# Optimization experiments

Hardware: AMD Instinct MI355X
Metric: run time of the kernel (lower is better)

## Reference

```python
import jax, jax.numpy as jnp
import numpy as np

NUM_HEADS = 12

def setup_inputs() -> dict:
    key = jax.random.key(0)
    ks = jax.random.split(key, 5)
    B, S, E = 1, 4096, 768
    x = jax.random.normal(ks[0], (B, S, E), dtype=jnp.float32)
    Wqkv = jax.random.normal(ks[1], (3 * E, E), dtype=jnp.float32) * (E ** -0.5)
    bqkv = jax.random.normal(ks[2], (3 * E,), dtype=jnp.float32) * 0.02
    Wo = jax.random.normal(ks[3], (E, E), dtype=jnp.float32) * (E ** -0.5)
    bo = jax.random.normal(ks[4], (E,), dtype=jnp.float32) * 0.02
    return {"x": x, "Wqkv": Wqkv, "bqkv": bqkv, "Wo": Wo, "bo": bo, "window_size": 128}

def reference(x, Wqkv, bqkv, Wo, bo, window_size):
    B, S, E = x.shape
    H = NUM_HEADS
    hd = E // H
    # qkv projection: [B,S,3E] -> [B,S,H,3*hd] -> split
    qkv = (x @ Wqkv.T + bqkv).reshape(B, S, H, 3 * hd)
    q, k, v = jnp.split(qkv, 3, axis=-1)  # each [B,S,H,hd]
    q = q.transpose(0, 2, 1, 3)  # [B,H,S,hd]
    k = k.transpose(0, 2, 1, 3)
    v = v.transpose(0, 2, 1, 3)
    # dense scores, masked to local window |i-j| <= window_size
    scores = jnp.einsum('bhqd,bhkd->bhqk', q, k) / (hd ** 0.5)
    idx = jnp.arange(S)
    in_window = jnp.abs(idx[:, None] - idx[None, :]) <= window_size  # [S,S]
    scores = jnp.where(in_window[None, None, :, :], scores, -jnp.inf)
    attn = jax.nn.softmax(scores, axis=-1)
    out = jnp.einsum('bhqk,bhkd->bhqd', attn, v)  # [B,H,S,hd]
    out = out.transpose(0, 2, 1, 3).reshape(B, S, E)
    return out @ Wo.T + bo
```

## Files before the change

### kernel.cpp

```cpp
#include <hip/hip_runtime.h>


typedef __attribute__((ext_vector_type(8))) short short8;
typedef __attribute__((ext_vector_type(4))) short short4v;
typedef __attribute__((ext_vector_type(4))) float f32x4;

#define S_LEN 4096
#define EMB   768
#define NH    12
#define HD    64
#define QT    64
#define WMAX  128
#define NKT   20
#define QSCALE 0.18033688f

#if defined(__HIP_DEVICE_COMPILE__)
#define MFMA16(a, b, c) __builtin_amdgcn_mfma_f32_16x16x16bf16_1k(a, b, c, 0, 0, 0)
#else
#define MFMA16(a, b, c) (c)
#endif

__device__ __forceinline__ short f2bf(float f) {
    union { unsigned int i; float f; } c;
    c.f = f;
    unsigned int i = c.i;
    unsigned int r = (i + 0x7FFFu + ((i >> 16) & 1u)) >> 16;
    return (short)(unsigned short)r;
}

#define NX4  (S_LEN * EMB / 4)
#define NW4  (3 * EMB * EMB / 4)
#define NO4  (EMB * EMB / 4)
__global__ __launch_bounds__(256) void convert_all(
    const float* __restrict__ x, const float* __restrict__ wqkv,
    const float* __restrict__ wo, short* __restrict__ xb,
    short* __restrict__ wqkvb, short* __restrict__ wob)
{
    int base = blockIdx.x * 1024 + threadIdx.x;
#pragma unroll
    for (int p = 0; p < 4; ++p) {
        int i = base + p * 256;
        const float* src; short* dst; int off;
        if (i < NX4)            { src = x;    dst = xb;    off = i; }
        else if (i < NX4 + NW4) { src = wqkv; dst = wqkvb; off = i - NX4; }
        else                    { src = wo;   dst = wob;   off = i - NX4 - NW4; }
        float4 v = ((const float4*)src)[off];
        short4v o = { f2bf(v.x), f2bf(v.y), f2bf(v.z), f2bf(v.w) };
        *(short4v*)(dst + (size_t)off * 4) = o;
    }
}

__global__ __launch_bounds__(256) void gemm_qkv(
    const short* __restrict__ A, const short* __restrict__ B,
    const float* __restrict__ bias, short* __restrict__ Cv,
    int M, int N, int K)
{
    __shared__ __align__(16) short smem[2 * 4096 + 2 * 3072];
    short* As0 = smem;
    short* Bs0 = smem + 2 * 4096;

    const int t = threadIdx.x;
    const int w = t >> 6, l = t & 63;
    const int quad = l >> 4, lane16 = l & 15;
    const int m0 = blockIdx.y * 128, n0 = blockIdx.x * 96;
    const int wm = (w >> 1) * 64, wn = (w & 1) * 48;

    f32x4 acc[4][3];
#pragma unroll
    for (int i = 0; i < 4; ++i)
#pragma unroll
        for (int j = 0; j < 3; ++j) acc[i][j] = (f32x4){0.f, 0.f, 0.f, 0.f};

    const int NKI = K >> 5;

    auto stage = [&](int ki, int b) {
        short* Asb = As0 + b * 4096;
        short* Bsb = Bs0 + b * 3072;
#pragma unroll
        for (int i = 0; i < 4; ++i) {
            int c = i * 256 + t;
            if (c < 512) {
                int r = c >> 2, kc = c & 3;
#if defined(__HIP_DEVICE_COMPILE__) && __has_builtin(__builtin_amdgcn_global_load_lds)
                __builtin_amdgcn_global_load_lds(
                    (const __attribute__((address_space(1))) void*)(A + (size_t)(m0 + r) * K + ki * 32 + kc * 8),
                    (__attribute__((address_space(3))) void*)(Asb + c * 8), 16, 0, 0);
#else
                *(short8*)(Asb + c * 8) = *(const short8*)(A + (size_t)(m0 + r) * K + ki * 32 + kc * 8);
#endif
            } else if (c < 896) {
                int cb = c - 512;
                int r = cb >> 2, kc = cb & 3;
#if defined(__HIP_DEVICE_COMPILE__) && __has_builtin(__builtin_amdgcn_global_load_lds)
                __builtin_amdgcn_global_load_lds(
                    (const __attribute__((address_space(1))) void*)(B + (size_t)(n0 + r) * K + ki * 32 + kc * 8),
                    (__attribute__((address_space(3))) void*)(Bsb + cb * 8), 16, 0, 0);
#else
                *(short8*)(Bsb + cb * 8) = *(const short8*)(B + (size_t)(n0 + r) * K + ki * 32 + kc * 8);
#endif
            }
        }
    };

    stage(0, 0);
    for (int kb = 0; kb < NKI; ++kb) {
        const int cur = kb & 1;
        __syncthreads();
        if (kb + 1 < NKI) stage(kb + 1, cur ^ 1);

        const short* Asb = As0 + cur * 4096;
        const short* Bsb = Bs0 + cur * 3072;
        short8 af[4], bfr[3];
#pragma unroll
        for (int mt = 0; mt < 4; ++mt)
            af[mt] = *(const short8*)(Asb + (wm + mt * 16 + lane16) * 32 + quad * 8);
#pragma unroll
        for (int nt = 0; nt < 3; ++nt)
            bfr[nt] = *(const short8*)(Bsb + (wn + nt * 16 + lane16) * 32 + quad * 8);
#pragma unroll
        for (int mt = 0; mt < 4; ++mt)
#pragma unroll
            for (int nt = 0; nt < 3; ++nt)
                acc[mt][nt] = __builtin_amdgcn_mfma_f32_16x16x32_bf16(
                    af[mt], bfr[nt], acc[mt][nt], 0, 0, 0);
    }

    __syncthreads();
    short(*Ct)[100] = (short(*)[100])smem;

#pragma unroll
    for (int nt = 0; nt < 3; ++nt) {
        int col = n0 + wn + nt * 16 + lane16;
        float bv = bias[col];
        int h = col / 192;
        int rem = col - h * 192;
        int ty = rem >> 6, d = rem & 63;
        if (ty == 2) {
            short* vt = Cv + ((size_t)2 * NH * S_LEN) * HD + ((size_t)h * HD + d) * S_LEN;
#pragma unroll
            for (int mt = 0; mt < 4; ++mt) {
                int row0 = m0 + wm + mt * 16 + quad * 4;
                short4v o = { f2bf(acc[mt][nt][0] + bv), f2bf(acc[mt][nt][1] + bv),
                              f2bf(acc[mt][nt][2] + bv), f2bf(acc[mt][nt][3] + bv) };
                *(short4v*)(vt + row0) = o;
            }
        } else {
            float s = (ty == 0) ? QSCALE : 1.f;
            int cl = wn + nt * 16 + lane16;
#pragma unroll
            for (int mt = 0; mt < 4; ++mt) {
#pragma unroll
                for (int r = 0; r < 4; ++r)
                    Ct[wm + mt * 16 + quad * 4 + r][cl] = f2bf((acc[mt][nt][r] + bv) * s);
            }
        }
    }
    __syncthreads();

#pragma unroll
    for (int pass = 0; pass < 6; ++pass) {
        int c = pass * 256 + t;
        int row = c / 12, cg = c - row * 12;
        int col0 = n0 + cg * 8;
        int h = col0 / 192;
        int rem = col0 - h * 192;
        int ty = rem >> 6;
        if (ty == 2) continue;
        int d0 = rem - ty * 64;
        short* dst = Cv + (((size_t)ty * NH + h) * S_LEN + (m0 + row)) * HD + d0;
        *(short8*)dst = *(const short8*)(&Ct[row][cg * 8]);
    }
}

__global__ __launch_bounds__(256, 3) void attn_win(
    const short* __restrict__ qsplit, const int* __restrict__ wptr,
    short* __restrict__ attn_out)
{
    __shared__ __align__(16) short KS[320 * 64];

    const int t = threadIdx.x;
    const int w = t >> 6, l = t & 63;
    const int quad = l >> 4, lane16 = l & 15;

    const int id = blockIdx.x;
    const int xcd = id & 7, j = id >> 3;
    const int h = j >> 3;
    const int q0 = ((xcd << 3) + (j & 7)) * QT;
    const int W = *wptr;
    const int kbase = q0 - WMAX;

    const short* Qh  = qsplit + (size_t)h * S_LEN * HD;
    const short* Kh  = qsplit + (size_t)(NH + h) * S_LEN * HD;
    const short* VtG = qsplit + (size_t)2 * NH * S_LEN * HD + (size_t)h * HD * S_LEN;

#pragma unroll
    for (int i = 0; i < 10; ++i) {
        int c = i * 256 + t;
        int r = c >> 3, gs = c & 7;
        int g = gs ^ (r & 7);
        int idx = min(max(kbase + r, 0), S_LEN - 1);
#if defined(__HIP_DEVICE_COMPILE__) && __has_builtin(__builtin_amdgcn_global_load_lds)
        __builtin_amdgcn_global_load_lds(
            (const __attribute__((address_space(1))) void*)(Kh + (size_t)idx * HD + g * 8),
            (__attribute__((address_space(3))) void*)(KS + c * 8), 16, 0, 0);
#else
        *(short8*)(KS + c * 8) = *(const short8*)(Kh + (size_t)idx * HD + g * 8);
#endif
    }
    const int qi = q0 + w * 16 + lane16;
    const short* qp = Qh + (size_t)qi * HD;
    short8 bq0 = *(const short8*)(qp + quad * 8);
    short8 bq1 = *(const short8*)(qp + 32 + quad * 8);

    __syncthreads();

    f32x4 sc[NKT];
    const int d7 = lane16 & 7;
    const int s0 = (quad ^ d7) * 8;
    const int s1 = ((quad + 4) ^ d7) * 8;
#pragma unroll
    for (int kt = 0; kt < NKT; ++kt) {
        const short* kp = KS + (kt * 16 + lane16) * 64;
        short8 a0 = *(const short8*)(kp + s0);
        short8 a1 = *(const short8*)(kp + s1);
        f32x4 a = (f32x4){0.f, 0.f, 0.f, 0.f};
        a = __builtin_amdgcn_mfma_f32_16x16x32_bf16(a0, bq0, a, 0, 0, 0);
        a = __builtin_amdgcn_mfma_f32_16x16x32_bf16(a1, bq1, a, 0, 0, 0);
        sc[kt] = a;
    }

    __syncthreads();

#pragma unroll
    for (int i = 0; i < 10; ++i) {
        int c = i * 256 + t;
        int d = c / 40;
        int slot = c - d * 40;
        int sg = slot >> 3, s = slot & 7;
        int g = s ^ (d & 7);
        int key0 = kbase + sg * 64 + g * 8;
        key0 = min(max(key0, 0), S_LEN - 8);
#if defined(__HIP_DEVICE_COMPILE__) && __has_builtin(__builtin_amdgcn_global_load_lds)
        __builtin_amdgcn_global_load_lds(
            (const __attribute__((address_space(1))) void*)(VtG + (size_t)d * S_LEN + key0),
            (__attribute__((address_space(3))) void*)(KS + c * 8), 16, 0, 0);
#else
        *(short8*)(KS + c * 8) = *(const short8*)(VtG + (size_t)d * S_LEN + key0);
#endif
    }

    float m = -1e30f;
#pragma unroll
    for (int kt = 0; kt < NKT; ++kt) {
#pragma unroll
        for (int r = 0; r < 4; ++r) {
            int key = kbase + kt * 16 + quad * 4 + r;
            int dd = qi - key;
            int ad = dd < 0 ? -dd : dd;
            bool valid = ((unsigned)key < S_LEN) && (ad <= W);
            float s = valid ? sc[kt][r] : -1e30f;
            sc[kt][r] = s;
            m = fmaxf(m, s);
        }
    }
    m = fmaxf(m, __shfl_xor(m, 16, 64));
    m = fmaxf(m, __shfl_xor(m, 32, 64));

    float lsum = 0.f;
#pragma unroll
    for (int kt = 0; kt < NKT; ++kt) {
#pragma unroll
        for (int r = 0; r < 4; ++r) {
            float p = exp2f(sc[kt][r] - m);
            sc[kt][r] = p;
            lsum += p;
        }
    }
    lsum += __shfl_xor(lsum, 16, 64);
    lsum += __shfl_xor(lsum, 32, 64);
    const float rl = 1.f / fmaxf(lsum, 1e-30f);

    __syncthreads();

    f32x4 oacc[4];
#pragma unroll
    for (int nt = 0; nt < 4; ++nt) oacc[nt] = (f32x4){0.f, 0.f, 0.f, 0.f};

#pragma unroll
    for (int kt = 0; kt < NKT; ++kt) {
        short4v pb = { f2bf(sc[kt][0]), f2bf(sc[kt][1]),
                       f2bf(sc[kt][2]), f2bf(sc[kt][3]) };
        int G = kt * 2 + (quad >> 1);
        int off = (G >> 3) * 64 + ((G & 7) ^ d7) * 8 + (quad & 1) * 4;
#pragma unroll
        for (int nt = 0; nt < 4; ++nt) {
            short4v va = *(const short4v*)(KS + (nt * 16 + lane16) * 320 + off);
            oacc[nt] = MFMA16(va, pb, oacc[nt]);
        }
    }

#pragma unroll
    for (int nt = 0; nt < 4; ++nt) {
        short4v ob = { f2bf(oacc[nt][0] * rl), f2bf(oacc[nt][1] * rl),
                       f2bf(oacc[nt][2] * rl), f2bf(oacc[nt][3] * rl) };
        *(short4v*)(attn_out + (size_t)qi * EMB + h * HD + nt * 16 + quad * 4) = ob;
    }
}

__global__ __launch_bounds__(256) void gemm_out96(
    const short* __restrict__ A, const short* __restrict__ B,
    const float* __restrict__ bias, float* __restrict__ C,
    int M, int N, int K)
{
    __shared__ __align__(16) short smem[2 * 4096 + 2 * 6144];
    short* As0 = smem;
    short* Bs0 = smem + 2 * 4096;

    const int t = threadIdx.x;
    const int w = t >> 6, l = t & 63;
    const int quad = l >> 4, lane16 = l & 15;
    const int m0 = blockIdx.y * 64, n0 = blockIdx.x * 96;
    const int wm = (w >> 1) * 32, wn = (w & 1) * 48;

    f32x4 acc[2][3];
#pragma unroll
    for (int i = 0; i < 2; ++i)
#pragma unroll
        for (int j = 0; j < 3; ++j) acc[i][j] = (f32x4){0.f, 0.f, 0.f, 0.f};

    const int NKI = K >> 6;

    auto stage = [&](int ki, int b) {
        short* Asb = As0 + b * 4096;
        short* Bsb = Bs0 + b * 6144;
#pragma unroll
        for (int i = 0; i < 5; ++i) {
            int c = i * 256 + t;
            if (c < 512) {
                int r = c >> 3, kc = c & 7;
                int g = kc ^ (r & 7);
#if defined(__HIP_DEVICE_COMPILE__) && __has_builtin(__builtin_amdgcn_global_load_lds)
                __builtin_amdgcn_global_load_lds(
                    (const __attribute__((address_space(1))) void*)(A + (size_t)(m0 + r) * K + ki * 64 + g * 8),
                    (__attribute__((address_space(3))) void*)(Asb + c * 8), 16, 0, 0);
#else
                *(short8*)(Asb + c * 8) = *(const short8*)(A + (size_t)(m0 + r) * K + ki * 64 + g * 8);
#endif
            } else {
                int cb = c - 512;
                int r = cb >> 3, kc = cb & 7;
                int g = kc ^ (r & 7);
#if defined(__HIP_DEVICE_COMPILE__) && __has_builtin(__builtin_amdgcn_global_load_lds)
                __builtin_amdgcn_global_load_lds(
                    (const __attribute__((address_space(1))) void*)(B + (size_t)(n0 + r) * K + ki * 64 + g * 8),
                    (__attribute__((address_space(3))) void*)(Bsb + cb * 8), 16, 0, 0);
#else
                *(short8*)(Bsb + cb * 8) = *(const short8*)(B + (size_t)(n0 + r) * K + ki * 64 + g * 8);
#endif
            }
        }
    };

    stage(0, 0);
    for (int kb = 0; kb < NKI; ++kb) {
        const int cur = kb & 1;
        __syncthreads();
        if (kb + 1 < NKI) stage(kb + 1, cur ^ 1);

        const short* Asb = As0 + cur * 4096;
        const short* Bsb = Bs0 + cur * 6144;
#pragma unroll
        for (int ks = 0; ks < 2; ++ks) {
            short8 af[2], bfr[3];
#pragma unroll
            for (int mt = 0; mt < 2; ++mt) {
                int row = wm + mt * 16 + lane16;
                int slot = (ks * 4 + quad) ^ (row & 7);
                af[mt] = *(const short8*)(Asb + row * 64 + slot * 8);
            }
#pragma unroll
            for (int nt = 0; nt < 3; ++nt) {
                int row = wn + nt * 16 + lane16;
                int slot = (ks * 4 + quad) ^ (row & 7);
                bfr[nt] = *(const short8*)(Bsb + row * 64 + slot * 8);
            }
#pragma unroll
            for (int mt = 0; mt < 2; ++mt)
#pragma unroll
                for (int nt = 0; nt < 3; ++nt)
                    acc[mt][nt] = __builtin_amdgcn_mfma_f32_16x16x32_bf16(
                        af[mt], bfr[nt], acc[mt][nt], 0, 0, 0);
        }
    }

    __syncthreads();
    float(*Ct)[100] = (float(*)[100])smem;

#pragma unroll
    for (int nt = 0; nt < 3; ++nt) {
        int cl = wn + nt * 16 + lane16;
        float bv = bias[n0 + cl];
#pragma unroll
        for (int mt = 0; mt < 2; ++mt) {
#pragma unroll
            for (int r = 0; r < 4; ++r)
                Ct[wm + mt * 16 + quad * 4 + r][cl] = acc[mt][nt][r] + bv;
        }
    }
    __syncthreads();

#pragma unroll
    for (int pass = 0; pass < 6; ++pass) {
        int c = pass * 256 + t;
        int row = c / 24, cg = c - row * 24;
        float4 v = { Ct[row][cg * 4], Ct[row][cg * 4 + 1],
                     Ct[row][cg * 4 + 2], Ct[row][cg * 4 + 3] };
        *(float4*)(C + (size_t)(m0 + row) * N + n0 + cg * 4) = v;
    }
}

extern "C" void kernel_launch(void* const* d_in, const int* in_sizes, int n_in,
                              void* d_out, int out_size, void* d_ws, size_t ws_size,
                              hipStream_t stream) {
    const float* x    = (const float*)d_in[0];
    const float* Wqkv = (const float*)d_in[1];
    const float* bqkv = (const float*)d_in[2];
    const float* Wo   = (const float*)d_in[3];
    const float* bo   = (const float*)d_in[4];
    const int*   wptr = (const int*)d_in[5];

    float* out = (float*)d_out;

    short* xb     = (short*)d_ws;
    short* wqkvb  = xb     + (size_t)S_LEN * EMB;
    short* wob    = wqkvb  + (size_t)3 * EMB * EMB;
    short* qsplit = wob    + (size_t)EMB * EMB;
    short* attn   = qsplit + (size_t)3 * NH * S_LEN * HD;

    dim3 blk(256);
    convert_all<<<dim3((NX4 + NW4 + NO4) / 1024), blk, 0, stream>>>(
        x, Wqkv, Wo, xb, wqkvb, wob);
    gemm_qkv<<<dim3(2304 / 96, S_LEN / 128), blk, 0, stream>>>(
        xb, wqkvb, bqkv, qsplit, S_LEN, 2304, EMB);
    attn_win<<<dim3(S_LEN / QT * NH), blk, 0, stream>>>(qsplit, wptr, attn);
    gemm_out96<<<dim3(EMB / 96, S_LEN / 64), blk, 0, stream>>>(
        attn, wob, bo, out, S_LEN, EMB, EMB);
}
```

Measured before the change: 134.1 us.

## Load GEMM weight fragments directly to registers and stage only A in LDS

After: 155.7 us. 16.1% more time.

```diff
diff --git a/kernel.cpp b/kernel.cpp
--- a/kernel.cpp
+++ b/kernel.cpp
@@ -55,9 +55,8 @@
     const float* __restrict__ bias, short* __restrict__ Cv,
     int M, int N, int K)
 {
-    __shared__ __align__(16) short smem[2 * 4096 + 2 * 3072];
+    __shared__ __align__(16) short smem[16384];
     short* As0 = smem;
-    short* Bs0 = smem + 2 * 4096;
 
     const int t = threadIdx.x;
     const int w = t >> 6, l = t & 63;
@@ -71,58 +70,80 @@
 #pragma unroll
         for (int j = 0; j < 3; ++j) acc[i][j] = (f32x4){0.f, 0.f, 0.f, 0.f};
 
-    const int NKI = K >> 5;
-
-    auto stage = [&](int ki, int b) {
-        short* Asb = As0 + b * 4096;
-        short* Bsb = Bs0 + b * 3072;
+    const int NKI = K >> 6;
+
+    const short* Bp0 = B + (size_t)(n0 + wn +  0 + lane16) * K + quad * 8;
+    const short* Bp1 = B + (size_t)(n0 + wn + 16 + lane16) * K + quad * 8;
+    const short* Bp2 = B + (size_t)(n0 + wn + 32 + lane16) * K + quad * 8;
+
+    auto stageA = [&](int ki, int b) {
+        short* Asb = As0 + b * 8192;
 #pragma unroll
         for (int i = 0; i < 4; ++i) {
             int c = i * 256 + t;
-            if (c < 512) {
-                int r = c >> 2, kc = c & 3;
+            int r = c >> 3, kc = c & 7;
+            int g = kc ^ (r & 7);
 #if defined(__HIP_DEVICE_COMPILE__) && __has_builtin(__builtin_amdgcn_global_load_lds)
-                __builtin_amdgcn_global_load_lds(
-                    (const __attribute__((address_space(1))) void*)(A + (size_t)(m0 + r) * K + ki * 32 + kc * 8),
-                    (__attribute__((address_space(3))) void*)(Asb + c * 8), 16, 0, 0);
+            __builtin_amdgcn_global_load_lds(
+                (const __attribute__((address_space(1))) void*)(A + (size_t)(m0 + r) * K + ki * 64 + g * 8),
+                (__attribute__((address_space(3))) void*)(Asb + c * 8), 16, 0, 0);
 #else
-                *(short8*)(Asb + c * 8) = *(const short8*)(A + (size_t)(m0 + r) * K + ki * 32 + kc * 8);
+            *(short8*)(Asb + c * 8) = *(const short8*)(A + (size_t)(m0 + r) * K + ki * 64 + g * 8);
 #endif
-            } else if (c < 896) {
-                int cb = c - 512;
-                int r = cb >> 2, kc = cb & 3;
-#if defined(__HIP_DEVICE_COMPILE__) && __has_builtin(__builtin_amdgcn_global_load_lds)
-                __builtin_amdgcn_global_load_lds(
-                    (const __attribute__((address_space(1))) void*)(B + (size_t)(n0 + r) * K + ki * 32 + kc * 8),
-                    (__attribute__((address_space(3))) void*)(Bsb + cb * 8), 16, 0, 0);
-#else
-                *(short8*)(Bsb + cb * 8) = *(const short8*)(B + (size_t)(n0 + r) * K + ki * 32 + kc * 8);
-#endif
-            }
         }
     };
 
-    stage(0, 0);
+    short8 bA0, bA1, bA2, bB0, bB1, bB2;
+    bA0 = *(const short8*)(Bp0);
+    bA1 = *(const short8*)(Bp1);
+    bA2 = *(const short8*)(Bp2);
+    stageA(0, 0);
+
     for (int kb = 0; kb < NKI; ++kb) {
         const int cur = kb & 1;
         __syncthreads();
-        if (kb + 1 < NKI) stage(kb + 1, cur ^ 1);
-
-        const short* Asb = As0 + cur * 4096;
-        const short* Bsb = Bs0 + cur * 3072;
-        short8 af[4], bfr[3];
-#pragma unroll
-        for (int mt = 0; mt < 4; ++mt)
-            af[mt] = *(const short8*)(Asb + (wm + mt * 16 + lane16) * 32 + quad * 8);
-#pragma unroll
-        for (int nt = 0; nt < 3; ++nt)
-            bfr[nt] = *(const short8*)(Bsb + (wn + nt * 16 + lane16) * 32 + quad * 8);
-#pragma unroll
-        for (int mt = 0; mt < 4; ++mt)
-#pragma unroll
-            for (int nt = 0; nt < 3; ++nt)
-                acc[mt][nt] = __builtin_amdgcn_mfma_f32_16x16x32_bf16(
-                    af[mt], bfr[nt], acc[mt][nt], 0, 0, 0);
+        if (kb + 1 < NKI) stageA(kb + 1, cur ^ 1);
+
+        const short* Asb = As0 + cur * 8192;
+
+        short8 af[4];
+#pragma unroll
+        for (int mt = 0; mt < 4; ++mt) {
+            int row = wm + mt * 16 + lane16;
+            int slot = quad ^ (row & 7);
+            af[mt] = *(const short8*)(Asb + row * 64 + slot * 8);
+        }
+        {
+            size_t o = (size_t)kb * 64 + 32;
+            bB0 = *(const short8*)(Bp0 + o);
+            bB1 = *(const short8*)(Bp1 + o);
+            bB2 = *(const short8*)(Bp2 + o);
+        }
+#pragma unroll
+        for (int mt = 0; mt < 4; ++mt) {
+            acc[mt][0] = __builtin_amdgcn_mfma_f32_16x16x32_bf16(af[mt], bA0, acc[mt][0], 0, 0, 0);
+            acc[mt][1] = __builtin_amdgcn_mfma_f32_16x16x32_bf16(af[mt], bA1, acc[mt][1], 0, 0, 0);
+            acc[mt][2] = __builtin_amdgcn_mfma_f32_16x16x32_bf16(af[mt], bA2, acc[mt][2], 0, 0, 0);
+        }
+
+#pragma unroll
+        for (int mt = 0; mt < 4; ++mt) {
+            int row = wm + mt * 16 + lane16;
+            int slot = (4 + quad) ^ (row & 7);
+            af[mt] = *(const short8*)(Asb + row * 64 + slot * 8);
+        }
+        {
+            size_t o = (size_t)(kb + 1 < NKI ? kb + 1 : 0) * 64;
+            bA0 = *(const short8*)(Bp0 + o);
+            bA1 = *(const short8*)(Bp1 + o);
+            bA2 = *(const short8*)(Bp2 + o);
+        }
+#pragma unroll
+        for (int mt = 0; mt < 4; ++mt) {
+            acc[mt][0] = __builtin_amdgcn_mfma_f32_16x16x32_bf16(af[mt], bB0, acc[mt][0], 0, 0, 0);
+            acc[mt][1] = __builtin_amdgcn_mfma_f32_16x16x32_bf16(af[mt], bB1, acc[mt][1], 0, 0, 0);
+            acc[mt][2] = __builtin_amdgcn_mfma_f32_16x16x32_bf16(af[mt], bB2, acc[mt][2], 0, 0, 0);
+        }
     }
 
     __syncthreads();
@@ -312,9 +333,8 @@
     const float* __restrict__ bias, float* __restrict__ C,
     int M, int N, int K)
 {
-    __shared__ __align__(16) short smem[2 * 4096 + 2 * 6144];
+    __shared__ __align__(16) short smem[12800];
     short* As0 = smem;
-    short* Bs0 = smem + 2 * 4096;
 
     const int t = threadIdx.x;
     const int w = t >> 6, l = t & 63;
@@ -330,66 +350,77 @@
 
     const int NKI = K >> 6;
 
-    auto stage = [&](int ki, int b) {
+    const short* Bp0 = B + (size_t)(n0 + wn +  0 + lane16) * K + quad * 8;
+    const short* Bp1 = B + (size_t)(n0 + wn + 16 + lane16) * K + quad * 8;
+    const short* Bp2 = B + (size_t)(n0 + wn + 32 + lane16) * K + quad * 8;
+
+    auto stageA = [&](int ki, int b) {
         short* Asb = As0 + b * 4096;
-        short* Bsb = Bs0 + b * 6144;
-#pragma unroll
-        for (int i = 0; i < 5; ++i) {
+#pragma unroll
+        for (int i = 0; i < 2; ++i) {
             int c = i * 256 + t;
-            if (c < 512) {
-                int r = c >> 3, kc = c & 7;
-                int g = kc ^ (r & 7);
+            int r = c >> 3, kc = c & 7;
+            int g = kc ^ (r & 7);
 #if defined(__HIP_DEVICE_COMPILE__) && __has_builtin(__builtin_amdgcn_global_load_lds)
-                __builtin_amdgcn_global_load_lds(
-                    (const __attribute__((address_space(1))) void*)(A + (size_t)(m0 + r) * K + ki * 64 + g * 8),
-                    (__attribute__((address_space(3))) void*)(Asb + c * 8), 16, 0, 0);
+            __builtin_amdgcn_global_load_lds(
+                (const __attribute__((address_space(1))) void*)(A + (size_t)(m0 + r) * K + ki * 64 + g * 8),
+                (__attribute__((address_space(3))) void*)(Asb + c * 8), 16, 0, 0);
 #else
-                *(short8*)(Asb + c * 8) = *(const short8*)(A + (size_t)(m0 + r) * K + ki * 64 + g * 8);
+            *(short8*)(Asb + c * 8) = *(const short8*)(A + (size_t)(m0 + r) * K + ki * 64 + g * 8);
 #endif
-            } else {
-                int cb = c - 512;
-                int r = cb >> 3, kc = cb & 7;
-                int g = kc ^ (r & 7);
-#if defined(__HIP_DEVICE_COMPILE__) && __has_builtin(__builtin_amdgcn_global_load_lds)
-                __builtin_amdgcn_global_load_lds(
-                    (const __attribute__((address_space(1))) void*)(B + (size_t)(n0 + r) * K + ki * 64 + g * 8),
-                    (__attribute__((address_space(3))) void*)(Bsb + cb * 8), 16, 0, 0);
-#else
-                *(short8*)(Bsb + cb * 8) = *(const short8*)(B + (size_t)(n0 + r) * K + ki * 64 + g * 8);
-#endif
-            }
         }
     };
 
-    stage(0, 0);
+    short8 bA0, bA1, bA2, bB0, bB1, bB2;
+    bA0 = *(const short8*)(Bp0);
+    bA1 = *(const short8*)(Bp1);
+    bA2 = *(const short8*)(Bp2);
+    stageA(0, 0);
+
     for (int kb = 0; kb < NKI; ++kb) {
         const int cur = kb & 1;
         __syncthreads();
-        if (kb + 1 < NKI) stage(kb + 1, cur ^ 1);
+        if (kb + 1 < NKI) stageA(kb + 1, cur ^ 1);
 
         const short* Asb = As0 + cur * 4096;
-        const short* Bsb = Bs0 + cur * 6144;
-#pragma unroll
-        for (int ks = 0; ks < 2; ++ks) {
-            short8 af[2], bfr[3];
-#pragma unroll
-            for (int mt = 0; mt < 2; ++mt) {
-                int row = wm + mt * 16 + lane16;
-                int slot = (ks * 4 + quad) ^ (row & 7);
-                af[mt] = *(const short8*)(Asb + row * 64 + slot * 8);
-            }
-#pragma unroll
-            for (int nt = 0; nt < 3; ++nt) {
-                int row = wn + nt * 16 + lane16;
-                int slot = (ks * 4 + quad) ^ (row & 7);
-                bfr[nt] = *(const short8*)(Bsb + row * 64 + slot * 8);
-            }
-#pragma unroll
-            for (int mt = 0; mt < 2; ++mt)
-#pragma unroll
-                for (int nt = 0; nt < 3; ++nt)
-                    acc[mt][nt] = __builtin_amdgcn_mfma_f32_16x16x32_bf16(
-                        af[mt], bfr[nt], acc[mt][nt], 0, 0, 0);
+
+        short8 af[2];
+#pragma unroll
+        for (int mt = 0; mt < 2; ++mt) {
+            int row = wm + mt * 16 + lane16;
+            int slot = quad ^ (row & 7);
+            af[mt] = *(const short8*)(Asb + row * 64 + slot * 8);
+        }
+        {
+            size_t o = (size_t)kb * 64 + 32;
+            bB0 = *(const short8*)(Bp0 + o);
+            bB1 = *(const short8*)(Bp1 + o);
+            bB2 = *(const short8*)(Bp2 + o);
+        }
+#pragma unroll
+        for (int mt = 0; mt < 2; ++mt) {
+            acc[mt][0] = __builtin_amdgcn_mfma_f32_16x16x32_bf16(af[mt], bA0, acc[mt][0], 0, 0, 0);
+            acc[mt][1] = __builtin_amdgcn_mfma_f32_16x16x32_bf16(af[mt], bA1, acc[mt][1], 0, 0, 0);
+            acc[mt][2] = __builtin_amdgcn_mfma_f32_16x16x32_bf16(af[mt], bA2, acc[mt][2], 0, 0, 0);
+        }
+
+#pragma unroll
+        for (int mt = 0; mt < 2; ++mt) {
+            int row = wm + mt * 16 + lane16;
+            int slot = (4 + quad) ^ (row & 7);
+            af[mt] = *(const short8*)(Asb + row * 64 + slot * 8);
+        }
+        {
+            size_t o = (size_t)(kb + 1 < NKI ? kb + 1 : 0) * 64;
+            bA0 = *(const short8*)(Bp0 + o);
+            bA1 = *(const short8*)(Bp1 + o);
+            bA2 = *(const short8*)(Bp2 + o);
+        }
+#pragma unroll
+        for (int mt = 0; mt < 2; ++mt) {
+            acc[mt][0] = __builtin_amdgcn_mfma_f32_16x16x32_bf16(af[mt], bB0, acc[mt][0], 0, 0, 0);
+            acc[mt][1] = __builtin_amdgcn_mfma_f32_16x16x32_bf16(af[mt], bB1, acc[mt][1], 0, 0, 0);
+            acc[mt][2] = __builtin_amdgcn_mfma_f32_16x16x32_bf16(af[mt], bB2, acc[mt][2], 0, 0, 0);
         }
     }
 
```
